# Performance work log

Measured on AMD Instinct MI355X. Metric: run time of the kernel, lower is better.

Reference implementation:

```python
import jax, jax.numpy as jnp
import numpy as np

WS = 4      # window size (hardcoded in original forward)
NH = 2      # num_head (module-level constant in original)


def _ln(x, g, b):
    mu = jnp.mean(x, axis=-1, keepdims=True)
    var = jnp.mean((x - mu) ** 2, axis=-1, keepdims=True)
    return (x - mu) * jax.lax.rsqrt(var + 1e-5) * g + b


def _img_to_win(img):
    # [B,H,W,D] -> [B, nW, WS*WS, D]  (matches F.unfold + reshape/transpose)
    B, H, W, D = img.shape
    s = H // WS
    x = img.reshape(B, s, WS, s, WS, D).transpose(0, 1, 3, 2, 4, 5)
    return x.reshape(B, s * s, WS * WS, D)


def _win_to_img(w):
    # [B, nW, WS*WS, D] -> [B,H,W,D]  (matches window2image)
    B, nW, P, D = w.shape
    s = int(np.sqrt(nW))
    x = w.reshape(B, s, s, WS, WS, D).transpose(0, 1, 3, 2, 4, 5)
    return x.reshape(B, s * WS, s * WS, D)


def _mhsa(x, wqkv, bqkv, wo, bo):
    # x: [B, S, D]; note: the original ignores additive_mask, so none is applied
    B, S, D = x.shape
    d = D // NH
    qkv = x @ wqkv.T + bqkv
    q, k, v = jnp.split(qkv, 3, axis=-1)
    q = q.reshape(B, S, NH, d).transpose(0, 2, 1, 3)
    k = k.reshape(B, S, NH, d).transpose(0, 2, 1, 3)
    v = v.reshape(B, S, NH, d).transpose(0, 2, 1, 3)
    p = jax.nn.softmax(jnp.einsum('bhqd,bhkd->bhqk', q, k) / np.sqrt(d).astype(np.float32), axis=-1)
    o = jnp.einsum('bhqk,bhkd->bhqd', p, v).transpose(0, 2, 1, 3).reshape(B, S, D)
    return o @ wo.T + bo


def _gelu(x):
    return jax.nn.gelu(x, approximate=False)


def setup_inputs() -> dict:
    key = jax.random.key(0)
    D = 128
    ks = jax.random.split(key, 16)
    w = lambda k, shp: (jax.random.normal(k, shp, dtype=jnp.float32) * 0.02)
    inp = {
        'x': jax.random.normal(ks[0], (8, 16384, D), dtype=jnp.float32),
        'ln1_g': jnp.ones((D,), jnp.float32), 'ln1_b': jnp.zeros((D,), jnp.float32),
        'ln2_g': jnp.ones((D,), jnp.float32), 'ln2_b': jnp.zeros((D,), jnp.float32),
        'ln3_g': jnp.ones((D,), jnp.float32), 'ln3_b': jnp.zeros((D,), jnp.float32),
        'ln4_g': jnp.ones((D,), jnp.float32), 'ln4_b': jnp.zeros((D,), jnp.float32),
        'qkv1_w': w(ks[1], (3 * D, D)), 'qkv1_b': jnp.zeros((3 * D,), jnp.float32),
        'out1_w': w(ks[2], (D, D)),     'out1_b': jnp.zeros((D,), jnp.float32),
        'qkv2_w': w(ks[3], (3 * D, D)), 'qkv2_b': jnp.zeros((3 * D,), jnp.float32),
        'out2_w': w(ks[4], (D, D)),     'out2_b': jnp.zeros((D,), jnp.float32),
        'mlp1_w1': w(ks[5], (4 * D, D)), 'mlp1_b1': jnp.zeros((4 * D,), jnp.float32),
        'mlp1_w2': w(ks[6], (D, 4 * D)), 'mlp1_b2': jnp.zeros((D,), jnp.float32),
        'mlp2_w1': w(ks[7], (4 * D, D)), 'mlp2_b1': jnp.zeros((4 * D,), jnp.float32),
        'mlp2_w2': w(ks[8], (D, 4 * D)), 'mlp2_b2': jnp.zeros((D,), jnp.float32),
    }
    return inp


def reference(x, ln1_g, ln1_b, ln2_g, ln2_b, ln3_g, ln3_b, ln4_g, ln4_b,
              qkv1_w, qkv1_b, out1_w, out1_b, qkv2_w, qkv2_b, out2_w, out2_b,
              mlp1_w1, mlp1_b1, mlp1_w2, mlp1_b2, mlp2_w1, mlp2_b1, mlp2_w2, mlp2_b2):
    B, N, D = x.shape
    H = int(np.sqrt(N))
    # --- W-MSA branch ---
    x1 = _ln(x, ln1_g, ln1_b)
    wins = _img_to_win(x1.reshape(B, H, H, D))            # [B,nW,P,D]
    nW, P = wins.shape[1], wins.shape[2]
    a1 = _mhsa(wins.reshape(B * nW, P, D), qkv1_w, qkv1_b, out1_w, out1_b)
    # original: input.long() -> truncate toward zero, detached; residual adds
    # window-order flattening (plain reshape, NOT window2image)
    res1 = jax.lax.stop_gradient(jnp.trunc(x)) + a1.reshape(B, N, D)
    h = _gelu(_ln(res1, ln2_g, ln2_b) @ mlp1_w1.T + mlp1_b1)
    h = _gelu(h @ mlp1_w2.T + mlp1_b2)
    out1 = h + res1
    # --- SW-MSA branch ---
    w2 = _ln(out1, ln3_g, ln3_b).reshape(B, nW, P, D)     # plain reshape (window order)
    img = jnp.roll(_win_to_img(w2), (-WS // 2, -WS // 2), axis=(1, 2))
    a2 = _mhsa(_img_to_win(img).reshape(B * nW, P, D), qkv2_w, qkv2_b, out2_w, out2_b)
    img2 = jnp.roll(_win_to_img(a2.reshape(B, nW, P, D)), (WS // 2, WS // 2), axis=(1, 2))
    res2 = out1 + _img_to_win(img2).reshape(B, N, D)      # plain reshape again
    h2 = _gelu(_ln(res2, ln4_g, ln4_b) @ mlp2_w1.T + mlp2_b1)
    h2 = _gelu(h2 @ mlp2_w2.T + mlp2_b2)
    out2 = h2 + res2
    return out2.reshape(B, nW, P, D)
```

## Files before the change

### kernel.cpp

```cpp
#include <hip/hip_runtime.h>


typedef unsigned short u16;
typedef unsigned int   u32;
typedef __attribute__((ext_vector_type(8))) short bf16x8;
typedef __attribute__((ext_vector_type(4))) float f32x4;

#define MFMA(a,b,c) __builtin_amdgcn_mfma_f32_16x16x32_bf16(a,b,c,0,0,0)

__device__ __forceinline__ u16 f2bf(float x) {
    u32 u = __float_as_uint(x);
    return (u16)((u + 0x7FFFu + ((u >> 16) & 1u)) >> 16);
}
__device__ __forceinline__ u32 pack2(float lo, float hi) {
    return (u32)f2bf(lo) | ((u32)f2bf(hi) << 16);
}
__device__ __forceinline__ float gelu_fast(float x) {
    float t = x * fmaf(x * x, 0.044715f, 1.0f);
    float e = __builtin_amdgcn_exp2f(-2.3022078f * t);
    return x * __builtin_amdgcn_rcpf(1.0f + e);
}
__device__ __forceinline__ bf16x8 ldsfrag(const u16* base, int byte) {
    return *(const bf16x8*)((const char*)base + byte);
}
__device__ __forceinline__ bf16x8 ldg8(const u16* __restrict__ p) {
    return *(const bf16x8*)p;
}
template <int BRANCH>
__device__ __forceinline__ int src_index(int wg, int tok) {
    int win = (wg << 2) + (tok >> 4), p = tok & 15;
    int r = ((win >> 5) << 2) | (p >> 2);
    int c = ((win & 31) << 2) | (p & 3);
    if (BRANCH == 1) return (r << 7) | c;
    int r2 = (r + 2) & 127, c2 = (c + 2) & 127;
    return ((((r2 >> 2) << 5) | (c2 >> 2)) << 4) | ((r2 & 3) << 2) | (c2 & 3);
}

__global__ __launch_bounds__(256)
void cvt_weights(const float* __restrict__ qkv1, const float* __restrict__ o1,
                 const float* __restrict__ w11,  const float* __restrict__ w12,
                 const float* __restrict__ qkv2, const float* __restrict__ o2,
                 const float* __restrict__ w21,  const float* __restrict__ w22,
                 u16* __restrict__ dst)
{
    int e = (blockIdx.x * 256 + threadIdx.x) * 8;
    const float* src; int off;
    if      (e < 49152)  { src = qkv1; off = 0; }
    else if (e < 65536)  { src = o1;   off = 49152; }
    else if (e < 131072) { src = w11;  off = 65536; }
    else if (e < 196608) { src = w12;  off = 131072; }
    else if (e < 245760) { src = qkv2; off = 196608; }
    else if (e < 262144) { src = o2;   off = 245760; }
    else if (e < 327680) { src = w21;  off = 262144; }
    else                 { src = w22;  off = 327680; }
    float4 a = *(const float4*)(src + (e - off));
    float4 b = *(const float4*)(src + (e - off) + 4);
    uint4 o;
    o.x = pack2(a.x, a.y); o.y = pack2(a.z, a.w);
    o.z = pack2(b.x, b.y); o.w = pack2(b.z, b.w);
    *(uint4*)(dst + e) = o;
}

template <int BRANCH>
__global__ __launch_bounds__(512, 4)
void swin_fused(const float* __restrict__ xin,
                const float* __restrict__ resin,
                float* __restrict__ resout,
                const float* __restrict__ lnA_g, const float* __restrict__ lnA_b,
                const float* __restrict__ lnB_g, const float* __restrict__ lnB_b,
                const u16* __restrict__ qkvw, const float* __restrict__ qkvb,
                const u16* __restrict__ ow,   const float* __restrict__ ob,
                const u16* __restrict__ w1,   const float* __restrict__ b1,
                const u16* __restrict__ w2,   const float* __restrict__ b2)
{
    __shared__ __align__(16) char smem[73728];
    u16*   xs   = (u16*)smem;
    u16*   qls  = (u16*)(smem + 16384);
    u16*   kls  = (u16*)(smem + 32768);
    u16*   vt   = (u16*)(smem + 49152);
    float* resf = (float*)(smem + 16384);
    u16*   h1   = (u16*)(smem + 49152);

    const int t  = threadIdx.x;
    const int wv = t >> 6, ln = t & 63, l15 = ln & 15, q4 = ln >> 4;
    const int bb = blockIdx.x >> 8, wg = blockIdx.x & 255;
    const int xa = (l15 & 7) << 4;
    const size_t gbase = (size_t)bb * 16384;

    {
        int token = t >> 3, part = t & 7;
        int nsrc = src_index<BRANCH>(wg, token);
        const float* src = xin + (gbase + nsrc) * 128;
        float v[16];
#pragma unroll
        for (int j = 0; j < 4; ++j)
            *(float4*)&v[j * 4] = *(const float4*)(src + part * 4 + 32 * j);
        float s = 0.f, s2 = 0.f;
#pragma unroll
        for (int i = 0; i < 16; ++i) { s += v[i]; s2 += v[i] * v[i]; }
        s  += __shfl_xor(s, 1, 8);  s  += __shfl_xor(s, 2, 8);  s  += __shfl_xor(s, 4, 8);
        s2 += __shfl_xor(s2, 1, 8); s2 += __shfl_xor(s2, 2, 8); s2 += __shfl_xor(s2, 4, 8);
        float mu = s * (1.f / 128.f);
        float rstd = rsqrtf(s2 * (1.f / 128.f) - mu * mu + 1e-5f);
        int xk = (token & 7) << 4;
#pragma unroll
        for (int j = 0; j < 4; ++j) {
            int d0 = part * 4 + 32 * j;
            float a0 = (v[j * 4 + 0] - mu) * rstd * lnA_g[d0]     + lnA_b[d0];
            float a1 = (v[j * 4 + 1] - mu) * rstd * lnA_g[d0 + 1] + lnA_b[d0 + 1];
            float a2 = (v[j * 4 + 2] - mu) * rstd * lnA_g[d0 + 2] + lnA_b[d0 + 2];
            float a3 = (v[j * 4 + 3] - mu) * rstd * lnA_g[d0 + 3] + lnA_b[d0 + 3];
            int byte = token * 256 + ((part * 8 + j * 64) ^ xk);
            *(uint2*)((char*)xs + byte) = make_uint2(pack2(a0, a1), pack2(a2, a3));
        }
        int row = t >> 2, slot = t & 3;
        int byte = row * 192 + ((128 + slot * 16) ^ ((row & 7) << 4));
        uint4 z = {0, 0, 0, 0};
        *(uint4*)((char*)vt + byte) = z;
    }
    __syncthreads();

#pragma unroll 1
    for (int i = 0; i < 3; ++i) {
        int n0 = (wv * 3 + i) * 16;
        int part = n0 >> 7, c0 = n0 & 127;
        float bias = qkvb[n0 + l15];
        f32x4 acc[4];
#pragma unroll
        for (int mf = 0; mf < 4; ++mf) acc[mf] = (f32x4){bias, bias, bias, bias};
#pragma unroll
        for (int kf = 0; kf < 4; ++kf) {
            bf16x8 bfr = ldg8(qkvw + (size_t)(n0 + l15) * 128 + kf * 32 + q4 * 8);
#pragma unroll
            for (int mf = 0; mf < 4; ++mf) {
                bf16x8 afr = ldsfrag(xs, (mf * 16 + l15) * 256 + ((kf * 64 + q4 * 16) ^ xa));
                acc[mf] = MFMA(afr, bfr, acc[mf]);
            }
        }
        if (part < 2) {
            u16* dst = part ? kls : qls;
            float sc = part ? 1.f : 0.125f;
#pragma unroll
            for (int mf = 0; mf < 4; ++mf)
#pragma unroll
                for (int r = 0; r < 4; ++r) {
                    int tok = mf * 16 + q4 * 4 + r;
                    int byte = tok * 256 + ((2 * (c0 + l15)) ^ ((tok & 7) << 4));
                    dst[byte >> 1] = f2bf(acc[mf][r] * sc);
                }
        } else {
            int dh = c0 + l15, xr = (dh & 7) << 4;
#pragma unroll
            for (int mf = 0; mf < 4; ++mf) {
                int tok0 = mf * 16 + q4 * 4;
                u32 lo = pack2(acc[mf][0], acc[mf][1]);
                u32 hi = pack2(acc[mf][2], acc[mf][3]);
                int byte = dh * 192 + ((2 * tok0) ^ xr);
                *(uint2*)((char*)vt + byte) = make_uint2(lo, hi);
            }
        }
    }
    __syncthreads();

    f32x4 S;
    {
        int win = wv >> 1, h = wv & 1;
        f32x4 z = {0.f, 0.f, 0.f, 0.f};
        int tok = win * 16 + l15, xk = (tok & 7) << 4;
#pragma unroll
        for (int kf = 0; kf < 2; ++kf) {
            int byte = tok * 256 + ((h * 128 + kf * 64 + q4 * 16) ^ xk);
            bf16x8 aq = ldsfrag(qls, byte);
            bf16x8 bk = ldsfrag(kls, byte);
            z = MFMA(aq, bk, z);
        }
        S = z;
    }
    __syncthreads();

    {
        int win = wv >> 1, h = wv & 1;
#pragma unroll
        for (int r = 0; r < 4; ++r) {
            float v = S[r];
            float m = v;
            m = fmaxf(m, __shfl_xor(m, 1, 16)); m = fmaxf(m, __shfl_xor(m, 2, 16));
            m = fmaxf(m, __shfl_xor(m, 4, 16)); m = fmaxf(m, __shfl_xor(m, 8, 16));
            float e = __builtin_amdgcn_exp2f((v - m) * 1.44269504f);
            float sm = e;
            sm += __shfl_xor(sm, 1, 16); sm += __shfl_xor(sm, 2, 16);
            sm += __shfl_xor(sm, 4, 16); sm += __shfl_xor(sm, 8, 16);
            float p = e * __builtin_amdgcn_rcpf(sm);
            int tok = win * 16 + q4 * 4 + r, xk = (tok & 7) << 4;
            qls[(tok * 128 + ((h * 64 + l15 * 2)      ^ xk)) >> 1] = f2bf(p);
            qls[(tok * 128 + ((h * 64 + 32 + l15 * 2) ^ xk)) >> 1] = 0;
        }
    }
    __syncthreads();

    {
        int win = wv >> 1, h = wv & 1;
        int atok = win * 16 + l15;
        bf16x8 ap = ldsfrag(qls, atok * 128 + ((h * 64 + q4 * 16) ^ ((atok & 7) << 4)));
#pragma unroll
        for (int nf = 0; nf < 4; ++nf) {
            int dh = h * 64 + nf * 16 + l15;
            bf16x8 bv = ldsfrag(vt, dh * 192 + ((win * 32 + q4 * 16) ^ ((dh & 7) << 4)));
            f32x4 z = {0.f, 0.f, 0.f, 0.f};
            f32x4 o = MFMA(ap, bv, z);
#pragma unroll
            for (int r = 0; r < 4; ++r) {
                int tok = win * 16 + q4 * 4 + r;
                xs[(tok * 256 + ((2 * dh) ^ ((tok & 7) << 4))) >> 1] = f2bf(o[r]);
            }
        }
    }
    __syncthreads();

    {
        int n0 = wv * 16;
        float bias = ob[n0 + l15];
        f32x4 acc[4];
#pragma unroll
        for (int mf = 0; mf < 4; ++mf) acc[mf] = (f32x4){bias, bias, bias, bias};
#pragma unroll
        for (int kf = 0; kf < 4; ++kf) {
            bf16x8 bfr = ldg8(ow + (size_t)(n0 + l15) * 128 + kf * 32 + q4 * 8);
#pragma unroll
            for (int mf = 0; mf < 4; ++mf) {
                bf16x8 afr = ldsfrag(xs, (mf * 16 + l15) * 256 + ((kf * 64 + q4 * 16) ^ xa));
                acc[mf] = MFMA(afr, bfr, acc[mf]);
            }
        }
#pragma unroll
        for (int mf = 0; mf < 4; ++mf)
#pragma unroll
            for (int r = 0; r < 4; ++r) {
                int tok = mf * 16 + q4 * 4 + r;
                int nd = (BRANCH == 1) ? (wg * 64 + tok) : src_index<2>(wg, tok);
                float rv = resin[(gbase + nd) * 128 + n0 + l15];
                if (BRANCH == 1) rv = truncf(rv);
                int byte = tok * 512 + ((4 * (n0 + l15)) ^ ((tok & 7) << 4));
                *(float*)((char*)resf + byte) = rv + acc[mf][r];
            }
    }
    __syncthreads();

    {
        int token = t >> 3, part = t & 7;
        int xk = (token & 7) << 4;
        float v[16];
#pragma unroll
        for (int j = 0; j < 4; ++j)
            *(float4*)&v[j * 4] =
                *(const float4*)((char*)resf + token * 512 + ((part * 16 + j * 128) ^ xk));
        float s = 0.f, s2 = 0.f;
#pragma unroll
        for (int i = 0; i < 16; ++i) { s += v[i]; s2 += v[i] * v[i]; }
        s  += __shfl_xor(s, 1, 8);  s  += __shfl_xor(s, 2, 8);  s  += __shfl_xor(s, 4, 8);
        s2 += __shfl_xor(s2, 1, 8); s2 += __shfl_xor(s2, 2, 8); s2 += __shfl_xor(s2, 4, 8);
        float mu = s * (1.f / 128.f);
        float rstd = rsqrtf(s2 * (1.f / 128.f) - mu * mu + 1e-5f);
#pragma unroll
        for (int j = 0; j < 4; ++j) {
            int d0 = part * 4 + 32 * j;
            float a0 = (v[j * 4 + 0] - mu) * rstd * lnB_g[d0]     + lnB_b[d0];
            float a1 = (v[j * 4 + 1] - mu) * rstd * lnB_g[d0 + 1] + lnB_b[d0 + 1];
            float a2 = (v[j * 4 + 2] - mu) * rstd * lnB_g[d0 + 2] + lnB_b[d0 + 2];
            float a3 = (v[j * 4 + 3] - mu) * rstd * lnB_g[d0 + 3] + lnB_b[d0 + 3];
            int byte = token * 256 + ((part * 8 + j * 64) ^ xk);
            *(uint2*)((char*)xs + byte) = make_uint2(pack2(a0, a1), pack2(a2, a3));
        }
    }
    __syncthreads();

    const int nm = wv * 16;
    f32x4 acc2[4];
    {
        float bias = b2[nm + l15];
#pragma unroll
        for (int mf = 0; mf < 4; ++mf) acc2[mf] = (f32x4){bias, bias, bias, bias};
    }
#pragma unroll 1
    for (int c = 0; c < 4; ++c) {
        f32x4 acc1[4];
        {
            float bias = b1[c * 128 + nm + l15];
#pragma unroll
            for (int mf = 0; mf < 4; ++mf) acc1[mf] = (f32x4){bias, bias, bias, bias};
        }
#pragma unroll
        for (int kf = 0; kf < 4; ++kf) {
            bf16x8 bfr = ldg8(w1 + (size_t)(c * 128 + nm + l15) * 128 + kf * 32 + q4 * 8);
#pragma unroll
            for (int mf = 0; mf < 4; ++mf) {
                bf16x8 afr = ldsfrag(xs, (mf * 16 + l15) * 256 + ((kf * 64 + q4 * 16) ^ xa));
                acc1[mf] = MFMA(afr, bfr, acc1[mf]);
            }
        }
        __syncthreads();
#pragma unroll
        for (int mf = 0; mf < 4; ++mf)
#pragma unroll
            for (int r = 0; r < 4; ++r) {
                int tok = mf * 16 + q4 * 4 + r;
                h1[(tok * 256 + ((2 * (nm + l15)) ^ ((tok & 7) << 4))) >> 1] =
                    f2bf(gelu_fast(acc1[mf][r]));
            }
        __syncthreads();
#pragma unroll
        for (int kf = 0; kf < 4; ++kf) {
            bf16x8 bfr = ldg8(w2 + (size_t)(nm + l15) * 512 + c * 128 + kf * 32 + q4 * 8);
#pragma unroll
            for (int mf = 0; mf < 4; ++mf) {
                bf16x8 afr = ldsfrag(h1, (mf * 16 + l15) * 256 + ((kf * 64 + q4 * 16) ^ xa));
                acc2[mf] = MFMA(afr, bfr, acc2[mf]);
            }
        }
    }

#pragma unroll
    for (int mf = 0; mf < 4; ++mf)
#pragma unroll
        for (int r = 0; r < 4; ++r) {
            int tok = mf * 16 + q4 * 4 + r;
            int nd = (BRANCH == 1) ? (wg * 64 + tok) : src_index<2>(wg, tok);
            float res = *(const float*)((char*)resf +
                            tok * 512 + ((4 * (nm + l15)) ^ ((tok & 7) << 4)));
            resout[(gbase + nd) * 128 + nm + l15] = gelu_fast(acc2[mf][r]) + res;
        }
}

extern "C" void kernel_launch(void* const* d_in, const int* in_sizes, int n_in,
                              void* d_out, int out_size, void* d_ws, size_t ws_size,
                              hipStream_t stream) {
    (void)in_sizes; (void)n_in; (void)out_size; (void)ws_size;
    const float* x      = (const float*)d_in[0];
    const float* ln1_g  = (const float*)d_in[1];
    const float* ln1_b  = (const float*)d_in[2];
    const float* ln2_g  = (const float*)d_in[3];
    const float* ln2_b  = (const float*)d_in[4];
    const float* ln3_g  = (const float*)d_in[5];
    const float* ln3_b  = (const float*)d_in[6];
    const float* ln4_g  = (const float*)d_in[7];
    const float* ln4_b  = (const float*)d_in[8];
    const float* qkv1_w = (const float*)d_in[9];
    const float* qkv1_b = (const float*)d_in[10];
    const float* out1_w = (const float*)d_in[11];
    const float* out1_b = (const float*)d_in[12];
    const float* qkv2_w = (const float*)d_in[13];
    const float* qkv2_b = (const float*)d_in[14];
    const float* out2_w = (const float*)d_in[15];
    const float* out2_b = (const float*)d_in[16];
    const float* mlp1_w1 = (const float*)d_in[17];
    const float* mlp1_b1 = (const float*)d_in[18];
    const float* mlp1_w2 = (const float*)d_in[19];
    const float* mlp1_b2 = (const float*)d_in[20];
    const float* mlp2_w1 = (const float*)d_in[21];
    const float* mlp2_b1 = (const float*)d_in[22];
    const float* mlp2_w2 = (const float*)d_in[23];
    const float* mlp2_b2 = (const float*)d_in[24];

    u16* wb = (u16*)d_ws;
    u16* qkv1bf = wb + 0;
    u16* out1bf = wb + 49152;
    u16* m1w1bf = wb + 65536;
    u16* m1w2bf = wb + 131072;
    u16* qkv2bf = wb + 196608;
    u16* out2bf = wb + 245760;
    u16* m2w1bf = wb + 262144;
    u16* m2w2bf = wb + 327680;

    float* out = (float*)d_out;

    cvt_weights<<<dim3(192), dim3(256), 0, stream>>>(
        qkv1_w, out1_w, mlp1_w1, mlp1_w2, qkv2_w, out2_w, mlp2_w1, mlp2_w2, wb);

    swin_fused<1><<<dim3(2048), dim3(512), 0, stream>>>(
        x, x, out,
        ln1_g, ln1_b, ln2_g, ln2_b,
        qkv1bf, qkv1_b, out1bf, out1_b,
        m1w1bf, mlp1_b1, m1w2bf, mlp1_b2);

    swin_fused<2><<<dim3(2048), dim3(512), 0, stream>>>(
        out, out, out,
        ln3_g, ln3_b, ln4_g, ln4_b,
        qkv2bf, qkv2_b, out2bf, out2_b,
        m2w1bf, mlp2_b1, m2w2bf, mlp2_b2);
}
```

Measured before the change: 278.1 us.

## Double-buffer MLP hidden tile, software-pipeline chunks, and prefetch weight fragments

```diff
diff --git a/kernel.cpp b/kernel.cpp
--- a/kernel.cpp
+++ b/kernel.cpp
@@ -1,4 +1,6 @@
 #include <hip/hip_runtime.h>
+#include <hip/hip_bf16.h>
+#include <string.h>
 
 
 typedef unsigned short u16;
@@ -9,11 +11,12 @@
 #define MFMA(a,b,c) __builtin_amdgcn_mfma_f32_16x16x32_bf16(a,b,c,0,0,0)
 
 __device__ __forceinline__ u16 f2bf(float x) {
-    u32 u = __float_as_uint(x);
-    return (u16)((u + 0x7FFFu + ((u >> 16) & 1u)) >> 16);
+    __hip_bfloat16 h = __float2bfloat16(x);
+    u16 r; memcpy(&r, &h, 2); return r;
 }
 __device__ __forceinline__ u32 pack2(float lo, float hi) {
-    return (u32)f2bf(lo) | ((u32)f2bf(hi) << 16);
+    __hip_bfloat162 h = __float22bfloat162_rn(make_float2(lo, hi));
+    u32 r; memcpy(&r, &h, 4); return r;
 }
 __device__ __forceinline__ float gelu_fast(float x) {
     float t = x * fmaf(x * x, 0.044715f, 1.0f);
@@ -73,13 +76,14 @@
                 const u16* __restrict__ w1,   const float* __restrict__ b1,
                 const u16* __restrict__ w2,   const float* __restrict__ b2)
 {
-    __shared__ __align__(16) char smem[73728];
+    __shared__ __align__(16) char smem[81920];
     u16*   xs   = (u16*)smem;
     u16*   qls  = (u16*)(smem + 16384);
     u16*   kls  = (u16*)(smem + 32768);
     u16*   vt   = (u16*)(smem + 49152);
     float* resf = (float*)(smem + 16384);
-    u16*   h1   = (u16*)(smem + 49152);
+    u16*   h1a  = (u16*)(smem + 49152);
+    u16*   h1b  = (u16*)(smem + 65536);
 
     const int t  = threadIdx.x;
     const int wv = t >> 6, ln = t & 63, l15 = ln & 15, q4 = ln >> 4;
@@ -113,10 +117,10 @@
             int byte = token * 256 + ((part * 8 + j * 64) ^ xk);
             *(uint2*)((char*)xs + byte) = make_uint2(pack2(a0, a1), pack2(a2, a3));
         }
-        int row = t >> 2, slot = t & 3;
-        int byte = row * 192 + ((128 + slot * 16) ^ ((row & 7) << 4));
+        int row = t >> 2, base = row * 256 + 128 + (t & 3) * 32;
         uint4 z = {0, 0, 0, 0};
-        *(uint4*)((char*)vt + byte) = z;
+        *(uint4*)((char*)vt + base)      = z;
+        *(uint4*)((char*)vt + base + 16) = z;
     }
     __syncthreads();
 
@@ -124,19 +128,21 @@
     for (int i = 0; i < 3; ++i) {
         int n0 = (wv * 3 + i) * 16;
         int part = n0 >> 7, c0 = n0 & 127;
+        bf16x8 wf[4];
+#pragma unroll
+        for (int kf = 0; kf < 4; ++kf)
+            wf[kf] = ldg8(qkvw + (size_t)(n0 + l15) * 128 + kf * 32 + q4 * 8);
         float bias = qkvb[n0 + l15];
         f32x4 acc[4];
 #pragma unroll
         for (int mf = 0; mf < 4; ++mf) acc[mf] = (f32x4){bias, bias, bias, bias};
 #pragma unroll
-        for (int kf = 0; kf < 4; ++kf) {
-            bf16x8 bfr = ldg8(qkvw + (size_t)(n0 + l15) * 128 + kf * 32 + q4 * 8);
+        for (int kf = 0; kf < 4; ++kf)
 #pragma unroll
             for (int mf = 0; mf < 4; ++mf) {
                 bf16x8 afr = ldsfrag(xs, (mf * 16 + l15) * 256 + ((kf * 64 + q4 * 16) ^ xa));
-                acc[mf] = MFMA(afr, bfr, acc[mf]);
-            }
-        }
+                acc[mf] = MFMA(afr, wf[kf], acc[mf]);
+            }
         if (part < 2) {
             u16* dst = part ? kls : qls;
             float sc = part ? 1.f : 0.125f;
@@ -155,7 +161,7 @@
                 int tok0 = mf * 16 + q4 * 4;
                 u32 lo = pack2(acc[mf][0], acc[mf][1]);
                 u32 hi = pack2(acc[mf][2], acc[mf][3]);
-                int byte = dh * 192 + ((2 * tok0) ^ xr);
+                int byte = dh * 256 + ((2 * tok0) ^ xr);
                 *(uint2*)((char*)vt + byte) = make_uint2(lo, hi);
             }
         }
@@ -205,7 +211,7 @@
 #pragma unroll
         for (int nf = 0; nf < 4; ++nf) {
             int dh = h * 64 + nf * 16 + l15;
-            bf16x8 bv = ldsfrag(vt, dh * 192 + ((win * 32 + q4 * 16) ^ ((dh & 7) << 4)));
+            bf16x8 bv = ldsfrag(vt, dh * 256 + ((win * 32 + q4 * 16) ^ ((dh & 7) << 4)));
             f32x4 z = {0.f, 0.f, 0.f, 0.f};
             f32x4 o = MFMA(ap, bv, z);
 #pragma unroll
@@ -219,19 +225,21 @@
 
     {
         int n0 = wv * 16;
+        bf16x8 wf[4];
+#pragma unroll
+        for (int kf = 0; kf < 4; ++kf)
+            wf[kf] = ldg8(ow + (size_t)(n0 + l15) * 128 + kf * 32 + q4 * 8);
         float bias = ob[n0 + l15];
         f32x4 acc[4];
 #pragma unroll
         for (int mf = 0; mf < 4; ++mf) acc[mf] = (f32x4){bias, bias, bias, bias};
 #pragma unroll
-        for (int kf = 0; kf < 4; ++kf) {
-            bf16x8 bfr = ldg8(ow + (size_t)(n0 + l15) * 128 + kf * 32 + q4 * 8);
+        for (int kf = 0; kf < 4; ++kf)
 #pragma unroll
             for (int mf = 0; mf < 4; ++mf) {
                 bf16x8 afr = ldsfrag(xs, (mf * 16 + l15) * 256 + ((kf * 64 + q4 * 16) ^ xa));
-                acc[mf] = MFMA(afr, bfr, acc[mf]);
-            }
-        }
+                acc[mf] = MFMA(afr, wf[kf], acc[mf]);
+            }
 #pragma unroll
         for (int mf = 0; mf < 4; ++mf)
 #pragma unroll
@@ -281,42 +289,83 @@
 #pragma unroll
         for (int mf = 0; mf < 4; ++mf) acc2[mf] = (f32x4){bias, bias, bias, bias};
     }
-#pragma unroll 1
-    for (int c = 0; c < 4; ++c) {
+    {
+        bf16x8 w1f[4];
+#pragma unroll
+        for (int kf = 0; kf < 4; ++kf)
+            w1f[kf] = ldg8(w1 + (size_t)(nm + l15) * 128 + kf * 32 + q4 * 8);
+        float bias = b1[nm + l15];
         f32x4 acc1[4];
-        {
-            float bias = b1[c * 128 + nm + l15];
-#pragma unroll
-            for (int mf = 0; mf < 4; ++mf) acc1[mf] = (f32x4){bias, bias, bias, bias};
-        }
-#pragma unroll
-        for (int kf = 0; kf < 4; ++kf) {
-            bf16x8 bfr = ldg8(w1 + (size_t)(c * 128 + nm + l15) * 128 + kf * 32 + q4 * 8);
+#pragma unroll
+        for (int mf = 0; mf < 4; ++mf) acc1[mf] = (f32x4){bias, bias, bias, bias};
+#pragma unroll
+        for (int kf = 0; kf < 4; ++kf)
 #pragma unroll
             for (int mf = 0; mf < 4; ++mf) {
                 bf16x8 afr = ldsfrag(xs, (mf * 16 + l15) * 256 + ((kf * 64 + q4 * 16) ^ xa));
-                acc1[mf] = MFMA(afr, bfr, acc1[mf]);
-            }
-        }
-        __syncthreads();
+                acc1[mf] = MFMA(afr, w1f[kf], acc1[mf]);
+            }
 #pragma unroll
         for (int mf = 0; mf < 4; ++mf)
 #pragma unroll
             for (int r = 0; r < 4; ++r) {
                 int tok = mf * 16 + q4 * 4 + r;
-                h1[(tok * 256 + ((2 * (nm + l15)) ^ ((tok & 7) << 4))) >> 1] =
+                h1a[(tok * 256 + ((2 * (nm + l15)) ^ ((tok & 7) << 4))) >> 1] =
                     f2bf(gelu_fast(acc1[mf][r]));
             }
+    }
+    __syncthreads();
+#pragma unroll 1
+    for (int c = 1; c < 4; ++c) {
+        u16* hcur  = (c & 1) ? h1b : h1a;
+        u16* hprev = (c & 1) ? h1a : h1b;
+        bf16x8 w1f[4], w2f[4];
+#pragma unroll
+        for (int kf = 0; kf < 4; ++kf)
+            w1f[kf] = ldg8(w1 + (size_t)(c * 128 + nm + l15) * 128 + kf * 32 + q4 * 8);
+#pragma unroll
+        for (int kf = 0; kf < 4; ++kf)
+            w2f[kf] = ldg8(w2 + (size_t)(nm + l15) * 512 + (c - 1) * 128 + kf * 32 + q4 * 8);
+#pragma unroll
+        for (int kf = 0; kf < 4; ++kf)
+#pragma unroll
+            for (int mf = 0; mf < 4; ++mf) {
+                bf16x8 afr = ldsfrag(hprev, (mf * 16 + l15) * 256 + ((kf * 64 + q4 * 16) ^ xa));
+                acc2[mf] = MFMA(afr, w2f[kf], acc2[mf]);
+            }
+        float bias = b1[c * 128 + nm + l15];
+        f32x4 acc1[4];
+#pragma unroll
+        for (int mf = 0; mf < 4; ++mf) acc1[mf] = (f32x4){bias, bias, bias, bias};
+#pragma unroll
+        for (int kf = 0; kf < 4; ++kf)
+#pragma unroll
+            for (int mf = 0; mf < 4; ++mf) {
+                bf16x8 afr = ldsfrag(xs, (mf * 16 + l15) * 256 + ((kf * 64 + q4 * 16) ^ xa));
+                acc1[mf] = MFMA(afr, w1f[kf], acc1[mf]);
+            }
+#pragma unroll
+        for (int mf = 0; mf < 4; ++mf)
+#pragma unroll
+            for (int r = 0; r < 4; ++r) {
+                int tok = mf * 16 + q4 * 4 + r;
+                hcur[(tok * 256 + ((2 * (nm + l15)) ^ ((tok & 7) << 4))) >> 1] =
+                    f2bf(gelu_fast(acc1[mf][r]));
+            }
         __syncthreads();
-#pragma unroll
-        for (int kf = 0; kf < 4; ++kf) {
-            bf16x8 bfr = ldg8(w2 + (size_t)(nm + l15) * 512 + c * 128 + kf * 32 + q4 * 8);
-#pragma unroll
-            for (int mf = 0; mf < 4; ++mf) {
-                bf16x8 afr = ldsfrag(h1, (mf * 16 + l15) * 256 + ((kf * 64 + q4 * 16) ^ xa));
-                acc2[mf] = MFMA(afr, bfr, acc2[mf]);
-            }
-        }
+    }
+    {
+        bf16x8 w2f[4];
+#pragma unroll
+        for (int kf = 0; kf < 4; ++kf)
+            w2f[kf] = ldg8(w2 + (size_t)(nm + l15) * 512 + 384 + kf * 32 + q4 * 8);
+#pragma unroll
+        for (int kf = 0; kf < 4; ++kf)
+#pragma unroll
+            for (int mf = 0; mf < 4; ++mf) {
+                bf16x8 afr = ldsfrag(h1b, (mf * 16 + l15) * 256 + ((kf * 64 + q4 * 16) ^ xa));
+                acc2[mf] = MFMA(afr, w2f[kf], acc2[mf]);
+            }
     }
 
 #pragma unroll
```

Result: slower. 356.6 us (+28.3%).
